# Optimization experiments

Hardware: AMD Instinct MI355X
Metric: run time of the kernel (lower is better)

Reference implementation:

```python
import jax, jax.numpy as jnp
import numpy as np

CLASS_NUM = 31
KERNEL_MUL = 2.0
KERNEL_NUM = 5


def setup_inputs() -> dict:
    key = jax.random.key(0)
    k1, k2, k3, k4 = jax.random.split(key, 4)
    S_total, T, D = 4096, 2048, 512
    return {
        "source": jax.random.normal(k1, (S_total, D), jnp.float32),
        "target": jax.random.normal(k2, (T, D), jnp.float32),
        "s_label": jax.random.randint(k3, (S_total,), 0, CLASS_NUM),
        "t_label": jax.random.normal(k4, (T, CLASS_NUM), jnp.float32),
        "num_source_data": 2048,
    }


def _mmd_loss(source, target, s_label, t_label, num_source_data):
    # Slice off the first num_source_data source rows (as in get_loss).
    src = source[num_source_data:]              # [S, D]
    s_lab = s_label[num_source_data:]           # [S]
    t_lab = jnp.argmax(t_label, axis=1)         # [T] hard target labels

    total = jnp.concatenate([src, target], axis=0)   # [N, D]
    # Full pairwise squared L2 distances, computed once and reused per class.
    sq = jnp.sum(total * total, axis=1)
    Dmat = jnp.maximum(sq[:, None] + sq[None, :] - 2.0 * (total @ total.T), 0.0)  # [N, N]

    dt = total.dtype
    loss = jnp.zeros((), dt)
    cnt = jnp.zeros((), dt)
    # Fixed small loop over class ids (mirrors the per-class python loop,
    # but uses masks instead of data-dependent boolean indexing for jit).
    for c in range(CLASS_NUM):
        ms = s_lab == c                          # [S] source mask
        mt = t_lab == c                          # [T] target mask
        m = jnp.concatenate([ms, mt]).astype(dt) # [N] pair membership
        # +1 for source rows, -1 for target rows: SS + TT - ST - TS
        sgn = jnp.concatenate([ms.astype(dt), -mt.astype(dt)])
        n = jnp.sum(m)                           # si + ti
        valid = (jnp.any(ms) & jnp.any(mt)).astype(dt)
        # median-heuristic bandwidth over the masked pairs (diag is 0)
        bw = (m @ Dmat @ m) / jnp.maximum(n * n - n, 1.0)
        bw = jnp.where(bw > 0, bw, 1.0) / (KERNEL_MUL ** (KERNEL_NUM // 2))
        K = sum(jnp.exp(-Dmat / (bw * KERNEL_MUL ** i)) for i in range(KERNEL_NUM))
        # sgn zeros out all entries outside the class-c block structure
        loss = loss + valid * (sgn @ K @ sgn) / jnp.maximum(n * n, 1.0)
        cnt = cnt + valid
    return loss / jnp.maximum(cnt, 1.0)


def reference(source, target, s_label, t_label, num_source_data):
    return _mmd_loss(source, target, s_label, t_label, num_source_data)
```

## Files before the change

### kernel.cpp

```cpp
#include <hip/hip_runtime.h>


#define CMAX 32
#define RCAP 6144
#define PCW 32
#define PAIR_Y 4

typedef __attribute__((ext_vector_type(8)))  short  short8;
typedef __attribute__((ext_vector_type(8)))  unsigned short ushort8;
typedef __attribute__((ext_vector_type(16))) float  float16;

__device__ inline unsigned short f2bf(float x) {
  unsigned u = __float_as_uint(x);
  return (unsigned short)((u + 0x7FFFu + ((u >> 16) & 1u)) >> 16);
}

__global__ __launch_bounds__(256) void k_fused(
    const float* __restrict__ src, const float* __restrict__ tgt,
    const int* __restrict__ slab, const float* __restrict__ tlabel,
    const int* __restrict__ nsd_p,
    int* pc,
    unsigned short* __restrict__ fragbuf,
    float* __restrict__ sqc, float* __restrict__ sgnc,
    int S_total, int T, int D, int C) {
  int lane = threadIdx.x & 63;
  int gwid = (blockIdx.x * 256 + threadIdx.x) >> 6;
  int nwv = (gridDim.x * 256) >> 6;
  int nsd = nsd_p[0];
  int S_use = S_total - nsd;
  int N = S_use + T;

  for (int r = gwid; r < N; r += nwv) {
    int c;
    const float* row;
    bool isSrc = (r < S_use);
    if (isSrc) {
      c = slab[nsd + r];
      row = src + (size_t)(nsd + r) * D;
    } else {
      int t = r - S_use;
      row = tgt + (size_t)t * D;
      float v = (lane < C) ? tlabel[(size_t)t * C + lane] : -3.4e38f;
      int idx = lane;
      for (int o = 16; o > 0; o >>= 1) {
        float ov = __shfl_down(v, o, 64);
        int oi = __shfl_down(idx, o, 64);
        if (ov > v || (ov == v && oi < idx)) { v = ov; idx = oi; }
      }
      c = __shfl(idx, 0, 64);
    }
    const float4* s4 = (const float4*)row;
    int nm = D >> 3;
    float4 v0, v1;
    if (lane < nm) { v0 = s4[lane * 2]; v1 = s4[lane * 2 + 1]; }

    int rk;
    if (lane == 0) rk = atomicAdd(&pc[c * PCW], 1);
    rk = __shfl(rk, 0, 64);
    int p = c * RCAP + rk;
    unsigned short* pb = fragbuf + (size_t)(c * RCAP + (rk & ~31)) * D;
    int row32 = rk & 31;

    float s = 0.f;
    if (lane < nm) {
      s += v0.x * v0.x + v0.y * v0.y + v0.z * v0.z + v0.w * v0.w +
           v1.x * v1.x + v1.y * v1.y + v1.z * v1.z + v1.w * v1.w;
      ushort8 h;
      h[0] = f2bf(v0.x); h[1] = f2bf(v0.y); h[2] = f2bf(v0.z); h[3] = f2bf(v0.w);
      h[4] = f2bf(v1.x); h[5] = f2bf(v1.y); h[6] = f2bf(v1.z); h[7] = f2bf(v1.w);
      int st = lane >> 1, hf = lane & 1;
      *(ushort8*)(pb + st * 512 + (hf * 32 + row32) * 8) = h;
    }
    for (int m = lane + 64; m < nm; m += 64) {
      float4 w0 = s4[m * 2], w1 = s4[m * 2 + 1];
      s += w0.x * w0.x + w0.y * w0.y + w0.z * w0.z + w0.w * w0.w +
           w1.x * w1.x + w1.y * w1.y + w1.z * w1.z + w1.w * w1.w;
      ushort8 h;
      h[0] = f2bf(w0.x); h[1] = f2bf(w0.y); h[2] = f2bf(w0.z); h[3] = f2bf(w0.w);
      h[4] = f2bf(w1.x); h[5] = f2bf(w1.y); h[6] = f2bf(w1.z); h[7] = f2bf(w1.w);
      int st = m >> 1, hf = m & 1;
      *(ushort8*)(pb + st * 512 + (hf * 32 + row32) * 8) = h;
    }
    for (int o = 32; o > 0; o >>= 1) s += __shfl_down(s, o, 64);
    if (lane == 0) {
      sqc[p] = s;
      sgnc[p] = isSrc ? 1.f : -1.f;
      atomicAdd((float*)&pc[(CMAX + c) * PCW], s);
      int* flag = &pc[(2 * CMAX + c) * PCW + (isSrc ? 0 : 1)];
      if (*(volatile int*)flag == 0) atomicExch(flag, 1);
    }
  }
}

__global__ __launch_bounds__(256) void k_pairs(
    const unsigned short* __restrict__ fragbuf, const float* __restrict__ sqc,
    const float* __restrict__ sgnc, const int* __restrict__ pc,
    float* losssum, int* done, float* __restrict__ out, int D, int C) {
  __shared__ float scs[4][64][8];
  __shared__ float s_inv0;
  __shared__ int lastFlag;
  int c = blockIdx.x;
  int tid = threadIdx.x;
  int n = pc[c * PCW];
  int off = c * RCAP;
  const unsigned short* base = fragbuf + (size_t)off * D;
  int nm = D >> 3;

  int rg = tid >> 6, cl = tid & 63;
  float nspart = 0.f;
  for (int m0 = 0; m0 < nm; m0 += 64) {
    int m = m0 + cl;
    float cs[8] = {0.f, 0.f, 0.f, 0.f, 0.f, 0.f, 0.f, 0.f};
    if (m < nm) {
      int st = m >> 1, hf = m & 1;
      for (int i = rg; i < n; i += 4) {
        ushort8 v = *(const ushort8*)(base + (size_t)(i & ~31) * D +
                                      st * 512 + (hf * 32 + (i & 31)) * 8);
        #pragma unroll
        for (int j = 0; j < 8; j++)
          cs[j] += __uint_as_float((unsigned)v[j] << 16);
      }
    }
    #pragma unroll
    for (int j = 0; j < 8; j++) scs[rg][cl][j] = cs[j];
    __syncthreads();
    if (tid < 64) {
      #pragma unroll
      for (int j = 0; j < 8; j++) {
        float t = scs[0][tid][j] + scs[1][tid][j] +
                  scs[2][tid][j] + scs[3][tid][j];
        nspart += t * t;
      }
    }
    __syncthreads();
  }
  if (tid < 64) {
    for (int o = 32; o > 0; o >>= 1) nspart += __shfl_down(nspart, o, 64);
    if (tid == 0) {
      float ss = ((const float*)pc)[(CMAX + c) * PCW];
      float nf = (float)n;
      float S1 = 2.f * nf * ss - 2.f * nspart;
      float bw = S1 / fmaxf(nf * nf - nf, 1.f);
      bw = (bw > 0.f) ? bw : 1.f;
      s_inv0 = 4.f / bw;
    }
  }
  __syncthreads();
  float inv0 = s_inv0;

  int tpr = (n + 31) >> 5;
  int tiles = tpr * (tpr + 1) / 2;
  int lane = tid & 63, l31 = lane & 31, half = lane >> 5;
  int wvc = blockIdx.y * 4 + (tid >> 6);
  int nwvc = gridDim.y * 4;
  float wsum = 0.f;

  for (int t = wvc; t < tiles; t += nwvc) {
    int lt = t, jt = 0;
    while (lt >= tpr - jt) { lt -= tpr - jt; jt++; }
    int kt = jt + lt;
    int jbase = jt << 5, kbase = kt << 5;
    float wgt = (jt == kt) ? 1.f : 2.f;

    float sqk  = sqc[off + kbase + l31];
    float sgk  = sgnc[off + kbase + l31];
    float sqjv = sqc[off + jbase + l31];
    float sgjv = sgnc[off + jbase + l31];
    bool kval = (kbase + l31) < n;

    const unsigned short* fa  = fragbuf + (size_t)(off + jbase) * D + lane * 8;
    const unsigned short* fbp = fragbuf + (size_t)(off + kbase) * D + lane * 8;
    float16 acc = {};
    if (D == 512) {
      #pragma unroll
      for (int s = 0; s < 32; s++) {
        short8 a = *(const short8*)(fa + s * 512);
        short8 b = *(const short8*)(fbp + s * 512);
        acc = __builtin_amdgcn_mfma_f32_32x32x16_bf16(a, b, acc, 0, 0, 0);
      }
    } else {
      for (int s = 0; s < (D >> 4); s++) {
        short8 a = *(const short8*)(fa + s * 512);
        short8 b = *(const short8*)(fbp + s * 512);
        acc = __builtin_amdgcn_mfma_f32_32x32x16_bf16(a, b, acc, 0, 0, 0);
      }
    }

    float contrib = 0.f;
    #pragma unroll
    for (int r = 0; r < 16; r++) {
      int m = (r & 3) + 8 * (r >> 2) + 4 * half;
      float sqj = __shfl(sqjv, m, 64);
      float sgj = __shfl(sgjv, m, 64);
      if (kval && (jbase + m) < n) {
        float d = fmaxf(sqj + sqk - 2.f * acc[r], 0.f);
        float s = inv0, kv = 0.f;
        #pragma unroll
        for (int q = 0; q < 5; q++) { kv += __expf(-d * s); s *= 0.5f; }
        contrib += sgj * sgk * kv;
      }
    }
    wsum += wgt * contrib;
  }
  for (int o = 32; o > 0; o >>= 1) wsum += __shfl_down(wsum, o, 64);
  if (lane == 0 && wsum != 0.f) atomicAdd(&losssum[c], wsum);

  __syncthreads();
  if (tid == 0) {
    __threadfence();
    int d = atomicAdd(done, 1);
    lastFlag = (d == (int)(gridDim.x * gridDim.y) - 1);
  }
  __syncthreads();
  if (lastFlag && tid < 64) {
    int cc = tid;
    float loss = 0.f, cv = 0.f;
    if (cc < C && pc[(2 * CMAX + cc) * PCW] > 0 &&
        pc[(2 * CMAX + cc) * PCW + 1] > 0) {
      float nf = (float)pc[cc * PCW];
      loss = atomicAdd(&losssum[cc], 0.f) / fmaxf(nf * nf, 1.f);
      cv = 1.f;
    }
    for (int o = 32; o > 0; o >>= 1) {
      loss += __shfl_down(loss, o, 64);
      cv   += __shfl_down(cv, o, 64);
    }
    if (tid == 0) out[0] = loss / fmaxf(cv, 1.f);
  }
}

extern "C" void kernel_launch(void* const* d_in, const int* in_sizes, int n_in,
                              void* d_out, int out_size, void* d_ws, size_t ws_size,
                              hipStream_t stream) {
  const float* source = (const float*)d_in[0];
  const float* target = (const float*)d_in[1];
  const int* slab     = (const int*)d_in[2];
  const float* tlabel = (const float*)d_in[3];
  const int* nsd_p    = (const int*)d_in[4];
  float* out = (float*)d_out;

  int S_total = in_sizes[2];
  int D = in_sizes[0] / S_total;
  int T = in_sizes[1] / D;
  int C = in_sizes[3] / T;

  int* ws = (int*)d_ws;
  int* pc       = ws;
  float* losssum = (float*)(ws + 3 * CMAX * PCW);
  int* done     = (int*)(losssum + C);
  int zwords    = 3 * CMAX * PCW + C + 8;

  float* sqc    = (float*)(ws + zwords);
  float* sgnc   = sqc + (size_t)C * RCAP;
  size_t words_used = (size_t)zwords + 2 * (size_t)C * RCAP;
  size_t fw = (words_used + 63) & ~(size_t)63;
  unsigned short* fragbuf = (unsigned short*)(ws + fw);

  hipMemsetAsync(d_ws, 0, (size_t)zwords * sizeof(int), stream);

  k_fused<<<1024, 256, 0, stream>>>(source, target, slab, tlabel, nsd_p,
                                    pc, fragbuf, sqc, sgnc,
                                    S_total, T, D, C);
  k_pairs<<<dim3(C, PAIR_Y), 256, 0, stream>>>(fragbuf, sqc, sgnc, pc,
                                               losssum, done, out, D, C);
}
```

Before: 95.66 us.

## Compute bandwidth from Gram tiles and keep MFMA accumulators across passes

The pairs kernel now runs one 1024-thread block per class instead of a 4-way split of 256-thread blocks. It derives the bandwidth's norm-of-sum term from the same MFMA Gram tiles it later uses for the kernel sum, replacing the separate column-sum pass over the fragments. When there are at most 32 tiles, each wave keeps its two accumulators in registers, so the Gram matrix is not recomputed. The per-class sum-of-squares and validity flags also move out of global atomics in the pack kernel into block reductions, at the cost of less parallelism per class and a bigger register footprint.

```diff
diff --git a/kernel.cpp b/kernel.cpp
--- a/kernel.cpp
+++ b/kernel.cpp
@@ -4,7 +4,8 @@
 #define CMAX 32
 #define RCAP 6144
 #define PCW 32
-#define PAIR_Y 4
+#define KP_THREADS 1024
+#define KP_WAVES 16
 
 typedef __attribute__((ext_vector_type(8)))  short  short8;
 typedef __attribute__((ext_vector_type(8)))  unsigned short ushort8;
@@ -85,147 +86,206 @@
     if (lane == 0) {
       sqc[p] = s;
       sgnc[p] = isSrc ? 1.f : -1.f;
-      atomicAdd((float*)&pc[(CMAX + c) * PCW], s);
-      int* flag = &pc[(2 * CMAX + c) * PCW + (isSrc ? 0 : 1)];
-      if (*(volatile int*)flag == 0) atomicExch(flag, 1);
-    }
-  }
-}
-
-__global__ __launch_bounds__(256) void k_pairs(
+    }
+  }
+}
+
+__device__ inline void tile_decode(int t, int tpr, int& jbase, int& kbase,
+                                   float& wgt) {
+  int lt = t, jt = 0;
+  while (lt >= tpr - jt) { lt -= tpr - jt; jt++; }
+  int kt = jt + lt;
+  jbase = jt << 5; kbase = kt << 5;
+  wgt = (jt == kt) ? 1.f : 2.f;
+}
+
+__device__ inline float16 tile_mfma(const unsigned short* __restrict__ fragbuf,
+                                    int off, int D, int jbase, int kbase,
+                                    int lane) {
+  const unsigned short* fa = fragbuf + (size_t)(off + jbase) * D + lane * 8;
+  const unsigned short* fb = fragbuf + (size_t)(off + kbase) * D + lane * 8;
+  float16 acc = {};
+  if (D == 512) {
+    #pragma unroll
+    for (int s = 0; s < 32; s++) {
+      short8 a = *(const short8*)(fa + s * 512);
+      short8 b = *(const short8*)(fb + s * 512);
+      acc = __builtin_amdgcn_mfma_f32_32x32x16_bf16(a, b, acc, 0, 0, 0);
+    }
+  } else {
+    for (int s = 0; s < (D >> 4); s++) {
+      short8 a = *(const short8*)(fa + s * 512);
+      short8 b = *(const short8*)(fb + s * 512);
+      acc = __builtin_amdgcn_mfma_f32_32x32x16_bf16(a, b, acc, 0, 0, 0);
+    }
+  }
+  return acc;
+}
+
+__device__ inline float ns_part(const float16& acc, int jbase, int kbase,
+                                int n, int l31, int half, float wgt) {
+  if ((kbase + l31) >= n) return 0.f;
+  float ps = 0.f;
+  #pragma unroll
+  for (int r = 0; r < 16; r++) {
+    int m = (r & 3) + 8 * (r >> 2) + 4 * half;
+    if ((jbase + m) < n) ps += acc[r];
+  }
+  return wgt * ps;
+}
+
+__device__ inline float tile_contrib(const float16& acc,
+                                     const float* __restrict__ sqc,
+                                     const float* __restrict__ sgnc,
+                                     int off, int jbase, int kbase, int n,
+                                     int l31, int half, float wgt, float inv0) {
+  float sqk  = sqc[off + kbase + l31];
+  float sgk  = sgnc[off + kbase + l31];
+  float sqjv = sqc[off + jbase + l31];
+  float sgjv = sgnc[off + jbase + l31];
+  bool kval = (kbase + l31) < n;
+  float contrib = 0.f;
+  #pragma unroll
+  for (int r = 0; r < 16; r++) {
+    int m = (r & 3) + 8 * (r >> 2) + 4 * half;
+    float sqj = __shfl(sqjv, m, 64);
+    float sgj = __shfl(sgjv, m, 64);
+    if (kval && (jbase + m) < n) {
+      float d = fmaxf(sqj + sqk - 2.f * acc[r], 0.f);
+      float s = inv0, kv = 0.f;
+      #pragma unroll
+      for (int q = 0; q < 5; q++) { kv += __expf(-d * s); s *= 0.5f; }
+      contrib += sgj * sgk * kv;
+    }
+  }
+  return wgt * contrib;
+}
+
+__global__ __launch_bounds__(KP_THREADS) void k_pairs(
     const unsigned short* __restrict__ fragbuf, const float* __restrict__ sqc,
     const float* __restrict__ sgnc, const int* __restrict__ pc,
-    float* losssum, int* done, float* __restrict__ out, int D, int C) {
-  __shared__ float scs[4][64][8];
+    float* losssum, float* glb ,
+    float* __restrict__ out, int D, int C) {
+  __shared__ float s_ns[KP_WAVES], s_ss[KP_WAVES], s_ws[KP_WAVES];
   __shared__ float s_inv0;
+  __shared__ int s_flag[2];
   __shared__ int lastFlag;
+
   int c = blockIdx.x;
   int tid = threadIdx.x;
+  int wv = tid >> 6, lane = tid & 63;
+  int l31 = lane & 31, half = lane >> 5;
   int n = pc[c * PCW];
   int off = c * RCAP;
-  const unsigned short* base = fragbuf + (size_t)off * D;
-  int nm = D >> 3;
-
-  int rg = tid >> 6, cl = tid & 63;
-  float nspart = 0.f;
-  for (int m0 = 0; m0 < nm; m0 += 64) {
-    int m = m0 + cl;
-    float cs[8] = {0.f, 0.f, 0.f, 0.f, 0.f, 0.f, 0.f, 0.f};
-    if (m < nm) {
-      int st = m >> 1, hf = m & 1;
-      for (int i = rg; i < n; i += 4) {
-        ushort8 v = *(const ushort8*)(base + (size_t)(i & ~31) * D +
-                                      st * 512 + (hf * 32 + (i & 31)) * 8);
-        #pragma unroll
-        for (int j = 0; j < 8; j++)
-          cs[j] += __uint_as_float((unsigned)v[j] << 16);
-      }
-    }
-    #pragma unroll
-    for (int j = 0; j < 8; j++) scs[rg][cl][j] = cs[j];
-    __syncthreads();
-    if (tid < 64) {
-      #pragma unroll
-      for (int j = 0; j < 8; j++) {
-        float t = scs[0][tid][j] + scs[1][tid][j] +
-                  scs[2][tid][j] + scs[3][tid][j];
-        nspart += t * t;
-      }
-    }
-    __syncthreads();
-  }
-  if (tid < 64) {
-    for (int o = 32; o > 0; o >>= 1) nspart += __shfl_down(nspart, o, 64);
-    if (tid == 0) {
-      float ss = ((const float*)pc)[(CMAX + c) * PCW];
-      float nf = (float)n;
-      float S1 = 2.f * nf * ss - 2.f * nspart;
-      float bw = S1 / fmaxf(nf * nf - nf, 1.f);
-      bw = (bw > 0.f) ? bw : 1.f;
-      s_inv0 = 4.f / bw;
-    }
-  }
-  __syncthreads();
-  float inv0 = s_inv0;
+
+  if (tid < 2) s_flag[tid] = 0;
+  __syncthreads();
+
+  float ssp = 0.f;
+  bool anyS = false, anyT = false;
+  for (int i = tid; i < n; i += KP_THREADS) {
+    ssp += sqc[off + i];
+    float g = sgnc[off + i];
+    anyS |= (g > 0.f); anyT |= (g < 0.f);
+  }
+  if (anyS) s_flag[0] = 1;
+  if (anyT) s_flag[1] = 1;
+  for (int o = 32; o > 0; o >>= 1) ssp += __shfl_down(ssp, o, 64);
+  if (lane == 0) s_ss[wv] = ssp;
 
   int tpr = (n + 31) >> 5;
   int tiles = tpr * (tpr + 1) / 2;
-  int lane = tid & 63, l31 = lane & 31, half = lane >> 5;
-  int wvc = blockIdx.y * 4 + (tid >> 6);
-  int nwvc = gridDim.y * 4;
+  bool fast = (tiles <= KP_WAVES * 2);
+
+  float16 accA = {}, accB = {};
+  int jbA = 0, kbA = 0, jbB = 0, kbB = 0;
+  float wgA = 0.f, wgB = 0.f;
+  bool hasA = false, hasB = false;
+  float nsp = 0.f;
+  if (fast) {
+    int tA = wv;
+    if (tA < tiles) {
+      tile_decode(tA, tpr, jbA, kbA, wgA);
+      accA = tile_mfma(fragbuf, off, D, jbA, kbA, lane);
+      nsp += ns_part(accA, jbA, kbA, n, l31, half, wgA);
+      hasA = true;
+    }
+    int tB = wv + KP_WAVES;
+    if (tB < tiles) {
+      tile_decode(tB, tpr, jbB, kbB, wgB);
+      accB = tile_mfma(fragbuf, off, D, jbB, kbB, lane);
+      nsp += ns_part(accB, jbB, kbB, n, l31, half, wgB);
+      hasB = true;
+    }
+  } else {
+    for (int t = wv; t < tiles; t += KP_WAVES) {
+      int jb, kb; float wg;
+      tile_decode(t, tpr, jb, kb, wg);
+      float16 acc = tile_mfma(fragbuf, off, D, jb, kb, lane);
+      nsp += ns_part(acc, jb, kb, n, l31, half, wg);
+    }
+  }
+  for (int o = 32; o > 0; o >>= 1) nsp += __shfl_down(nsp, o, 64);
+  if (lane == 0) s_ns[wv] = nsp;
+  __syncthreads();
+
+  if (tid == 0) {
+    float ss = 0.f, ns = 0.f;
+    #pragma unroll
+    for (int w = 0; w < KP_WAVES; w++) { ss += s_ss[w]; ns += s_ns[w]; }
+    float nf = (float)n;
+    float S1 = 2.f * nf * ss - 2.f * ns;
+    float bw = S1 / fmaxf(nf * nf - nf, 1.f);
+    bw = (bw > 0.f) ? bw : 1.f;
+    s_inv0 = 4.f / bw;
+  }
+  __syncthreads();
+  float inv0 = s_inv0;
+
   float wsum = 0.f;
-
-  for (int t = wvc; t < tiles; t += nwvc) {
-    int lt = t, jt = 0;
-    while (lt >= tpr - jt) { lt -= tpr - jt; jt++; }
-    int kt = jt + lt;
-    int jbase = jt << 5, kbase = kt << 5;
-    float wgt = (jt == kt) ? 1.f : 2.f;
-
-    float sqk  = sqc[off + kbase + l31];
-    float sgk  = sgnc[off + kbase + l31];
-    float sqjv = sqc[off + jbase + l31];
-    float sgjv = sgnc[off + jbase + l31];
-    bool kval = (kbase + l31) < n;
-
-    const unsigned short* fa  = fragbuf + (size_t)(off + jbase) * D + lane * 8;
-    const unsigned short* fbp = fragbuf + (size_t)(off + kbase) * D + lane * 8;
-    float16 acc = {};
-    if (D == 512) {
-      #pragma unroll
-      for (int s = 0; s < 32; s++) {
-        short8 a = *(const short8*)(fa + s * 512);
-        short8 b = *(const short8*)(fbp + s * 512);
-        acc = __builtin_amdgcn_mfma_f32_32x32x16_bf16(a, b, acc, 0, 0, 0);
-      }
-    } else {
-      for (int s = 0; s < (D >> 4); s++) {
-        short8 a = *(const short8*)(fa + s * 512);
-        short8 b = *(const short8*)(fbp + s * 512);
-        acc = __builtin_amdgcn_mfma_f32_32x32x16_bf16(a, b, acc, 0, 0, 0);
-      }
-    }
-
-    float contrib = 0.f;
+  if (fast) {
+    if (hasA) wsum += tile_contrib(accA, sqc, sgnc, off, jbA, kbA, n,
+                                   l31, half, wgA, inv0);
+    if (hasB) wsum += tile_contrib(accB, sqc, sgnc, off, jbB, kbB, n,
+                                   l31, half, wgB, inv0);
+  } else {
+    for (int t = wv; t < tiles; t += KP_WAVES) {
+      int jb, kb; float wg;
+      tile_decode(t, tpr, jb, kb, wg);
+      float16 acc = tile_mfma(fragbuf, off, D, jb, kb, lane);
+      wsum += tile_contrib(acc, sqc, sgnc, off, jb, kb, n,
+                           l31, half, wg, inv0);
+    }
+  }
+  for (int o = 32; o > 0; o >>= 1) wsum += __shfl_down(wsum, o, 64);
+  if (lane == 0) s_ws[wv] = wsum;
+  __syncthreads();
+
+  if (tid == 0) {
+    float tot = 0.f;
     #pragma unroll
-    for (int r = 0; r < 16; r++) {
-      int m = (r & 3) + 8 * (r >> 2) + 4 * half;
-      float sqj = __shfl(sqjv, m, 64);
-      float sgj = __shfl(sgjv, m, 64);
-      if (kval && (jbase + m) < n) {
-        float d = fmaxf(sqj + sqk - 2.f * acc[r], 0.f);
-        float s = inv0, kv = 0.f;
-        #pragma unroll
-        for (int q = 0; q < 5; q++) { kv += __expf(-d * s); s *= 0.5f; }
-        contrib += sgj * sgk * kv;
-      }
-    }
-    wsum += wgt * contrib;
-  }
-  for (int o = 32; o > 0; o >>= 1) wsum += __shfl_down(wsum, o, 64);
-  if (lane == 0 && wsum != 0.f) atomicAdd(&losssum[c], wsum);
+    for (int w = 0; w < KP_WAVES; w++) tot += s_ws[w];
+    bool valid = s_flag[0] && s_flag[1];
+    float nf = (float)n;
+    atomicExch(&losssum[c], valid ? tot / fmaxf(nf * nf, 1.f) : 0.f);
+    if (valid) atomicAdd(&glb[0], 1.f);
+  }
 
   __syncthreads();
   if (tid == 0) {
     __threadfence();
-    int d = atomicAdd(done, 1);
-    lastFlag = (d == (int)(gridDim.x * gridDim.y) - 1);
+    int d = atomicAdd((int*)&glb[1], 1);
+    lastFlag = (d == C - 1);
   }
   __syncthreads();
   if (lastFlag && tid < 64) {
     int cc = tid;
-    float loss = 0.f, cv = 0.f;
-    if (cc < C && pc[(2 * CMAX + cc) * PCW] > 0 &&
-        pc[(2 * CMAX + cc) * PCW + 1] > 0) {
-      float nf = (float)pc[cc * PCW];
-      loss = atomicAdd(&losssum[cc], 0.f) / fmaxf(nf * nf, 1.f);
-      cv = 1.f;
-    }
-    for (int o = 32; o > 0; o >>= 1) {
-      loss += __shfl_down(loss, o, 64);
-      cv   += __shfl_down(cv, o, 64);
-    }
-    if (tid == 0) out[0] = loss / fmaxf(cv, 1.f);
+    float loss = (cc < C) ? atomicAdd(&losssum[cc], 0.f) : 0.f;
+    for (int o = 32; o > 0; o >>= 1) loss += __shfl_down(loss, o, 64);
+    if (tid == 0) {
+      float cv = atomicAdd(&glb[0], 0.f);
+      out[0] = loss / fmaxf(cv, 1.f);
+    }
   }
 }
 
@@ -245,10 +305,10 @@
   int C = in_sizes[3] / T;
 
   int* ws = (int*)d_ws;
-  int* pc       = ws;
-  float* losssum = (float*)(ws + 3 * CMAX * PCW);
-  int* done     = (int*)(losssum + C);
-  int zwords    = 3 * CMAX * PCW + C + 8;
+  int* pc        = ws;
+  float* losssum = (float*)(ws + CMAX * PCW);
+  float* glb     = (float*)(ws + CMAX * PCW + CMAX);
+  int zwords     = CMAX * PCW + CMAX + 8;
 
   float* sqc    = (float*)(ws + zwords);
   float* sgnc   = sqc + (size_t)C * RCAP;
@@ -261,6 +321,6 @@
   k_fused<<<1024, 256, 0, stream>>>(source, target, slab, tlabel, nsd_p,
                                     pc, fragbuf, sqc, sgnc,
                                     S_total, T, D, C);
-  k_pairs<<<dim3(C, PAIR_Y), 256, 0, stream>>>(fragbuf, sqc, sgnc, pc,
-                                               losssum, done, out, D, C);
-}
+  k_pairs<<<C, KP_THREADS, 0, stream>>>(fragbuf, sqc, sgnc, pc,
+                                        losssum, glb, out, D, C);
+}
```

Result: faster. 86.69 us (-9.4%).
